# Kernel tuning notes

Hardware: AMD Instinct MI355X
Metric: run time of the kernel (lower is better)

Reference implementation:

```python
import jax, jax.numpy as jnp
import numpy as np

N_NODES = 65536
N_EDGES = 1048576
F_IN = 128
HEADS = 4
HID = 64
N_GRAPHS = 1024
NODES_PER_GRAPH = N_NODES // N_GRAPHS
EPS = 1e-5
NEG_SLOPE = 0.2


def setup_inputs() -> dict:
    key = jax.random.key(0)
    ks = jax.random.split(key, 8)
    x = jax.random.normal(ks[0], (N_NODES, F_IN), dtype=jnp.float32)
    edge_index = jax.random.randint(ks[1], (2, N_EDGES), 0, N_NODES, dtype=jnp.int64)
    batch = (jnp.arange(N_NODES, dtype=jnp.int64) // NODES_PER_GRAPH)
    s = 1.0 / np.sqrt(F_IN)
    w_l = jax.random.normal(ks[2], (HEADS * HID, F_IN), dtype=jnp.float32) * s
    w_r = jax.random.normal(ks[3], (HEADS * HID, F_IN), dtype=jnp.float32) * s
    att = jax.random.normal(ks[4], (HEADS, HID), dtype=jnp.float32) * (1.0 / np.sqrt(HID))
    return {
        "x": x,
        "edge_index": edge_index,
        "batch": batch,
        "num_graphs": N_GRAPHS,
        "bn_gamma": jnp.ones((F_IN,), jnp.float32),
        "bn_beta": jnp.zeros((F_IN,), jnp.float32),
        "w_l": w_l,
        "b_l": jnp.zeros((HEADS * HID,), jnp.float32),
        "w_r": w_r,
        "b_r": jnp.zeros((HEADS * HID,), jnp.float32),
        "att": att,
        "bias": jnp.zeros((HID,), jnp.float32),
    }


def reference(x, edge_index, batch, num_graphs, bn_gamma, bn_beta,
              w_l, b_l, w_r, b_r, att, bias):
    N = x.shape[0]
    H, C = att.shape
    # BatchNorm1d (training-mode: batch stats, biased variance)
    mean = jnp.mean(x, axis=0)
    var = jnp.var(x, axis=0)
    xn = (x - mean) * jax.lax.rsqrt(var + EPS) * bn_gamma + bn_beta
    # GATv2Conv: separate src/dst linear transforms
    xs = (xn @ w_l.T + b_l).reshape(N, H, C)
    xd = (xn @ w_r.T + b_r).reshape(N, H, C)
    # add self-loops (PyG default)
    loop = jnp.arange(N, dtype=edge_index.dtype)
    src = jnp.concatenate([edge_index[0], loop])
    dst = jnp.concatenate([edge_index[1], loop])
    # per-edge messages and GATv2 attention logits
    msg = xs[src]                               # [E, H, C]
    e = jax.nn.leaky_relu(msg + xd[dst], NEG_SLOPE)
    logits = jnp.einsum('ehc,hc->eh', e, att)    # [E, H]
    # segment-wise (per-destination) softmax
    m = jax.ops.segment_max(logits, dst, num_segments=N)
    p = jnp.exp(logits - m[dst])
    s = jax.ops.segment_sum(p, dst, num_segments=N)
    alpha = p / s[dst]                           # [E, H]
    # scatter-aggregate weighted messages
    out = jax.ops.segment_sum(alpha[:, :, None] * msg, dst, num_segments=N)  # [N,H,C]
    out = out.mean(axis=1) + bias                # concat=False -> mean over heads
    out = jax.nn.elu(out)
    return out.reshape(num_graphs, -1, C)
```

## Files before the change

### kernel.cpp

```cpp
#include <hip/hip_runtime.h>
#include <hip/hip_bf16.h>

#define N_NODES 65536
#define N_EDGES 1048576
#define F_IN    128
#define HEADS   4
#define HID     64
#define NHID    256
#define NBUCK   1024
#define BCAP    2048

typedef float fx4 __attribute__((ext_vector_type(4)));
typedef short bf16x8 __attribute__((ext_vector_type(8)));
typedef float f32x4 __attribute__((ext_vector_type(4)));

__device__ inline unsigned short f2bf(float f) {
    unsigned u = __float_as_uint(f);
    u += 0x7fff + ((u >> 16) & 1);
    return (unsigned short)(u >> 16);
}
__device__ inline float bf2f(unsigned short h) {
    return __uint_as_float((unsigned)h << 16);
}
__device__ inline float bflo(unsigned w) { return __uint_as_float(w << 16); }
__device__ inline float bfhi(unsigned w) { return __uint_as_float(w & 0xffff0000u); }

template <int CTRL>
__device__ inline float dpp_add(float x) {
    int y = __builtin_amdgcn_update_dpp(0, __float_as_int(x), CTRL, 0xf, 0xf, true);
    return x + __int_as_float(y);
}

__global__ __launch_bounds__(256) void k_bn_stats(const float* __restrict__ x,
                                                  float* __restrict__ sums,
                                                  unsigned short* __restrict__ xhi) {
    const int t = threadIdx.x;
    const int lane = t & 63;
    const int w = t >> 6;
    const int wid = blockIdx.x * 4 + w;
    float s0 = 0.f, s1 = 0.f, q0 = 0.f, q1 = 0.f;
    for (int i = 0; i < 64; ++i) {
        int r = wid + i * 1024;
        float2 v = *(const float2*)(x + (size_t)r * F_IN + lane * 2);
        s0 += v.x; q0 += v.x * v.x;
        s1 += v.y; q1 += v.y * v.y;
        unsigned short h0 = f2bf(v.x), h1 = f2bf(v.y);
        int slot = (lane >> 2) ^ (r & 7);
        int idx = r * 64 + slot * 4 + (lane & 3);
        ((unsigned*)xhi)[idx] = (unsigned)h0 | ((unsigned)h1 << 16);
    }
    __shared__ float sh[4][128];
    sh[w][lane * 2] = s0; sh[w][lane * 2 + 1] = s1;
    __syncthreads();
    if (t < 128) atomicAdd(&sums[t], sh[0][t] + sh[1][t] + sh[2][t] + sh[3][t]);
    __syncthreads();
    sh[w][lane * 2] = q0; sh[w][lane * 2 + 1] = q1;
    __syncthreads();
    if (t < 128) atomicAdd(&sums[128 + t], sh[0][t] + sh[1][t] + sh[2][t] + sh[3][t]);
}

__global__ void k_bn_finalize(const float* __restrict__ sums,
                              const float* __restrict__ gamma,
                              const float* __restrict__ beta,
                              const float* __restrict__ att,
                              float* __restrict__ scale,
                              float* __restrict__ shift,
                              float* __restrict__ att_l2e) {
    int t = threadIdx.x;
    float mean = sums[t] * (1.0f / N_NODES);
    float var  = sums[128 + t] * (1.0f / N_NODES) - mean * mean;
    float sc = gamma[t] * rsqrtf(var + 1e-5f);
    scale[t] = sc;
    shift[t] = beta[t] - mean * sc;
    att_l2e[t]       = att[t]       * 1.44269504088896f;
    att_l2e[t + 128] = att[t + 128] * 1.44269504088896f;
}

__global__ __launch_bounds__(256) void k_prep_w(const float* __restrict__ w_l,
                                                const float* __restrict__ b_l,
                                                const float* __restrict__ w_r,
                                                const float* __restrict__ b_r,
                                                const float* __restrict__ scale,
                                                const float* __restrict__ shift,
                                                unsigned short* __restrict__ Whi,
                                                unsigned short* __restrict__ Wlo,
                                                float* __restrict__ bp) {
    const int t = threadIdx.x;
    const int lane = t & 63;
    const int o = blockIdx.x * 4 + (t >> 6);
    const float* wrow = (o < NHID) ? (w_l + (size_t)o * F_IN)
                                   : (w_r + (size_t)(o - NHID) * F_IN);
    float bo = (o < NHID) ? b_l[o] : b_r[o - NHID];
    float2 wv = *(const float2*)(wrow + lane * 2);
    float w0 = wv.x * scale[lane * 2], w1 = wv.y * scale[lane * 2 + 1];
    unsigned short h0 = f2bf(w0), h1 = f2bf(w1);
    unsigned short l0 = f2bf(w0 - bf2f(h0)), l1 = f2bf(w1 - bf2f(h1));
    int slot = (lane >> 2) ^ (o & 7);
    int idx = o * 64 + slot * 4 + (lane & 3);
    ((unsigned*)Whi)[idx] = (unsigned)h0 | ((unsigned)h1 << 16);
    ((unsigned*)Wlo)[idx] = (unsigned)l0 | ((unsigned)l1 << 16);
    float part = shift[lane * 2] * wv.x + shift[lane * 2 + 1] * wv.y;
    #pragma unroll
    for (int m = 1; m < 64; m <<= 1) part += __shfl_xor(part, m, 64);
    if (lane == 0) bp[o] = bo + part;
}

__global__ __launch_bounds__(512) void k_gemm_mfma(const unsigned short* __restrict__ xhi,
                                                   const unsigned short* __restrict__ Whi,
                                                   const unsigned short* __restrict__ Wlo,
                                                   const float* __restrict__ bp,
                                                   unsigned short* __restrict__ xs_bf,
                                                   unsigned short* __restrict__ xd_bf) {
    __shared__ __align__(16) char lds[98304];
    const int t = threadIdx.x;
    const int bid = blockIdx.x;
    const int mb = (bid & 7) * 64 + ((bid >> 3) >> 2);
    const int nb = (bid >> 3) & 3;
    const int m0 = mb * 128, n0 = nb * 128;
    {
        const uint4* srcs[3] = {
            (const uint4*)(xhi + (size_t)m0 * 128),
            (const uint4*)(Whi + (size_t)n0 * 128),
            (const uint4*)(Wlo + (size_t)n0 * 128)};
        #pragma unroll
        for (int c = 0; c < 3; ++c) {
            uint4* dst = (uint4*)(lds + c * 32768);
            #pragma unroll
            for (int q = 0; q < 4; ++q) {
                int i = q * 512 + t;
                dst[i] = srcs[c][i];
            }
        }
    }
    __syncthreads();
    const int wvi = t >> 6, lane = t & 63;
    const int wm = wvi >> 2, wn = wvi & 3;
    const int lg = lane >> 4, lr = lane & 15;
    f32x4 acc[4][2] = {};
    #pragma unroll
    for (int ks = 0; ks < 4; ++ks) {
        bf16x8 ah[4], bh[2], bl[2];
        #pragma unroll
        for (int mi = 0; mi < 4; ++mi) {
            int r = wm * 64 + mi * 16 + lr;
            int off = r * 256 + ((((ks << 2) + lg) ^ (r & 7)) << 4);
            ah[mi] = *(const bf16x8*)(lds + off);
        }
        #pragma unroll
        for (int nj = 0; nj < 2; ++nj) {
            int r = wn * 32 + nj * 16 + lr;
            int off = r * 256 + ((((ks << 2) + lg) ^ (r & 7)) << 4);
            bh[nj] = *(const bf16x8*)(lds + 32768 + off);
            bl[nj] = *(const bf16x8*)(lds + 65536 + off);
        }
        #pragma unroll
        for (int mi = 0; mi < 4; ++mi)
            #pragma unroll
            for (int nj = 0; nj < 2; ++nj) {
                acc[mi][nj] = __builtin_amdgcn_mfma_f32_16x16x32_bf16(ah[mi], bh[nj], acc[mi][nj], 0, 0, 0);
                acc[mi][nj] = __builtin_amdgcn_mfma_f32_16x16x32_bf16(ah[mi], bl[nj], acc[mi][nj], 0, 0, 0);
            }
    }
    unsigned short* outp = (n0 < NHID) ? xs_bf : xd_bf;
    const int ncol0 = n0 & 255;
    #pragma unroll
    for (int nj = 0; nj < 2; ++nj) {
        int nc = wn * 32 + nj * 16 + lr;
        float bcol = bp[n0 + nc];
        #pragma unroll
        for (int mi = 0; mi < 4; ++mi) {
            #pragma unroll
            for (int r = 0; r < 4; ++r) {
                int m = m0 + wm * 64 + mi * 16 + lg * 4 + r;
                outp[(size_t)m * NHID + ncol0 + nc] = f2bf(acc[mi][nj][r] + bcol);
            }
        }
    }
}

__global__ __launch_bounds__(256) void k_coarse(const int* __restrict__ ei,
                                                int* __restrict__ ccnt,
                                                unsigned* __restrict__ cbuf) {
    __shared__ int cnt[NBUCK];
    __shared__ int base[NBUCK];
    const int t = threadIdx.x;
    for (int i = t; i < NBUCK; i += 256) cnt[i] = 0;
    __syncthreads();
    const int e0 = blockIdx.x * 4096;
    int myrank[16];
    #pragma unroll
    for (int k = 0; k < 16; ++k) {
        int d = ei[N_EDGES + e0 + k * 256 + t];
        myrank[k] = atomicAdd(&cnt[d >> 6], 1);
    }
    __syncthreads();
    for (int i = t; i < NBUCK; i += 256)
        base[i] = (i << 11) + atomicAdd(&ccnt[i], cnt[i]);
    __syncthreads();
    #pragma unroll
    for (int k = 0; k < 16; ++k) {
        int e = e0 + k * 256 + t;
        int s = ei[e];
        int d = ei[N_EDGES + e];
        unsigned pos = (unsigned)(base[d >> 6] + myrank[k]);
        if ((pos >> 11) == (unsigned)(d >> 6))
            cbuf[pos] = (unsigned)s | ((unsigned)(d & 63) << 16);
    }
}

__global__ __launch_bounds__(256) void k_fineA(const unsigned* __restrict__ cbuf,
                                               const int* __restrict__ ccnt,
                                               int* __restrict__ counts) {
    __shared__ int nc[64];
    const int t = threadIdx.x;
    const int b = blockIdx.x;
    if (t < 64) nc[t] = 0;
    __syncthreads();
    const int cnt = min(ccnt[b], BCAP);
    const unsigned* p = cbuf + (size_t)b * BCAP;
    for (int e = t; e < cnt; e += 256)
        atomicAdd(&nc[(p[e] >> 16) & 63], 1);
    __syncthreads();
    if (t < 64) counts[b * 64 + t] = nc[t];
}

__global__ __launch_bounds__(256) void k_scan1(const int* __restrict__ counts,
                                               int* __restrict__ row_start,
                                               int* __restrict__ blocksums) {
    __shared__ int sh[256];
    int t = threadIdx.x;
    int i = blockIdx.x * 256 + t;
    int v = counts[i];
    sh[t] = v;
    __syncthreads();
    for (int off = 1; off < 256; off <<= 1) {
        int add = (t >= off) ? sh[t - off] : 0;
        __syncthreads();
        sh[t] += add;
        __syncthreads();
    }
    row_start[i] = sh[t] - v;
    if (t == 255) blocksums[blockIdx.x] = sh[255];
}

__global__ void k_scan2(int* __restrict__ blocksums) {
    __shared__ int sh[256];
    int t = threadIdx.x;
    int v = blocksums[t];
    sh[t] = v;
    __syncthreads();
    for (int off = 1; off < 256; off <<= 1) {
        int add = (t >= off) ? sh[t - off] : 0;
        __syncthreads();
        sh[t] += add;
        __syncthreads();
    }
    blocksums[t] = sh[t] - v;
}

__global__ __launch_bounds__(256) void k_scan3(int* __restrict__ row_start,
                                               const int* __restrict__ blocksums) {
    int i = blockIdx.x * 256 + threadIdx.x;
    row_start[i] += blocksums[blockIdx.x];
}

__global__ __launch_bounds__(256) void k_fineB(const unsigned* __restrict__ cbuf,
                                               const int* __restrict__ ccnt,
                                               const int* __restrict__ row_start,
                                               int* __restrict__ csr) {
    __shared__ int rs[64];
    __shared__ int cur[64];
    const int t = threadIdx.x;
    const int b = blockIdx.x;
    if (t < 64) { rs[t] = row_start[b * 64 + t]; cur[t] = 0; }
    __syncthreads();
    const int cnt = min(ccnt[b], BCAP);
    const unsigned* p = cbuf + (size_t)b * BCAP;
    for (int e = t; e < cnt; e += 256) {
        unsigned w2 = p[e];
        int d = (w2 >> 16) & 63;
        int r = atomicAdd(&cur[d], 1);
        csr[rs[d] + r] = (int)(w2 & 0xffffu);
    }
}

__global__ __launch_bounds__(256, 4) void k_aggregate(const unsigned short* __restrict__ xs_bf,
                                                      const unsigned short* __restrict__ xd_bf,
                                                      const int* __restrict__ row_start,
                                                      const int* __restrict__ counts,
                                                      const int* __restrict__ csr,
                                                      const float* __restrict__ att_l2e,
                                                      const float* __restrict__ bias,
                                                      float* __restrict__ out) {
    const int t = threadIdx.x;
    const int lane = t & 63;
    const int q = lane & 31;
    const int h = lane >> 5;
    const int node  = __builtin_amdgcn_readfirstlane(blockIdx.x * 4 + (t >> 6));
    const int start = __builtin_amdgcn_readfirstlane(row_start[node]);
    const int deg   = __builtin_amdgcn_readfirstlane(counts[node]);
    const int total = deg + 1;
    const int* csrp = csr + start;

    float att8[8], xd8[8];
    {
        const float4* ap = (const float4*)(att_l2e + q * 8);
        float4 a0 = ap[0], a1 = ap[1];
        att8[0] = a0.x; att8[1] = a0.y; att8[2] = a0.z; att8[3] = a0.w;
        att8[4] = a1.x; att8[5] = a1.y; att8[6] = a1.z; att8[7] = a1.w;
        uint4 xw = *(const uint4*)(xd_bf + (size_t)node * NHID + q * 8);
        xd8[0] = bflo(xw.x); xd8[1] = bfhi(xw.x);
        xd8[2] = bflo(xw.y); xd8[3] = bfhi(xw.y);
        xd8[4] = bflo(xw.z); xd8[5] = bfhi(xw.z);
        xd8[6] = bflo(xw.w); xd8[7] = bfhi(xw.w);
    }

    const char* xsb = (const char*)xs_bf;
    const unsigned voff = (unsigned)q * 16;
    float ssum = 0.f;
    float acc[8] = {};

    int sA = node;
    int it1 = (1 < total) ? 1 : 0;
    int sB = (it1 == 0) ? node : csrp[it1 - 1];
    int srcv = h ? sB : sA;
    uint4 u = *(const uint4*)(xsb + (((unsigned)srcv << 9) | voff));

    for (int j = 0; j < total; j += 2) {
        uint4 cur = u;
        int jn = j + 2;
        if (jn < total) {
            int nA = csrp[jn - 1];
            int jB = (jn + 1 < total) ? jn + 1 : jn;
            int nB = csrp[jB - 1];
            int nsrc = h ? nB : nA;
            u = *(const uint4*)(xsb + (((unsigned)nsrc << 9) | voff));
        }
        float c0 = bflo(cur.x), c1 = bfhi(cur.x);
        float c2 = bflo(cur.y), c3 = bfhi(cur.y);
        float c4 = bflo(cur.z), c5 = bfhi(cur.z);
        float c6 = bflo(cur.w), c7 = bfhi(cur.w);
        float sv0 = c0 + xd8[0], sv1 = c1 + xd8[1];
        float sv2 = c2 + xd8[2], sv3 = c3 + xd8[3];
        float sv4 = c4 + xd8[4], sv5 = c5 + xd8[5];
        float sv6 = c6 + xd8[6], sv7 = c7 + xd8[7];
        float l0 = fmaxf(sv0, 0.2f * sv0), l1 = fmaxf(sv1, 0.2f * sv1);
        float l2 = fmaxf(sv2, 0.2f * sv2), l3 = fmaxf(sv3, 0.2f * sv3);
        float l4 = fmaxf(sv4, 0.2f * sv4), l5 = fmaxf(sv5, 0.2f * sv5);
        float l6 = fmaxf(sv6, 0.2f * sv6), l7 = fmaxf(sv7, 0.2f * sv7);
        float d = att8[0] * l0;
        d = fmaf(att8[1], l1, d); d = fmaf(att8[2], l2, d);
        d = fmaf(att8[3], l3, d); d = fmaf(att8[4], l4, d);
        d = fmaf(att8[5], l5, d); d = fmaf(att8[6], l6, d);
        d = fmaf(att8[7], l7, d);
        d = dpp_add<0xB1>(d);
        d = dpp_add<0x4E>(d);
        d = dpp_add<0x141>(d);
        if (j + h >= total) d = -1e30f;
        float p = __builtin_amdgcn_exp2f(d);
        ssum += p;
        acc[0] = fmaf(p, sv0, acc[0]); acc[1] = fmaf(p, sv1, acc[1]);
        acc[2] = fmaf(p, sv2, acc[2]); acc[3] = fmaf(p, sv3, acc[3]);
        acc[4] = fmaf(p, sv4, acc[4]); acc[5] = fmaf(p, sv5, acc[5]);
        acc[6] = fmaf(p, sv6, acc[6]); acc[7] = fmaf(p, sv7, acc[7]);
    }

    ssum += __shfl_xor(ssum, 32, 64);
    #pragma unroll
    for (int k = 0; k < 8; ++k) acc[k] += __shfl_xor(acc[k], 32, 64);
    float inv = __builtin_amdgcn_rcpf(ssum);
    float r[8];
    #pragma unroll
    for (int k = 0; k < 8; ++k) r[k] = fmaf(acc[k], inv, -xd8[k]);
    #pragma unroll
    for (int k = 0; k < 8; ++k) {
        r[k] += __shfl_xor(r[k], 8, 64);
        r[k] += __shfl_xor(r[k], 16, 64);
    }
    if (h == 0 && q < 8) {
        const float4* bp4 = (const float4*)(bias + q * 8);
        float4 b0 = bp4[0], b1 = bp4[1];
        float o[8];
        o[0] = r[0] * 0.25f + b0.x; o[1] = r[1] * 0.25f + b0.y;
        o[2] = r[2] * 0.25f + b0.z; o[3] = r[3] * 0.25f + b0.w;
        o[4] = r[4] * 0.25f + b1.x; o[5] = r[5] * 0.25f + b1.y;
        o[6] = r[6] * 0.25f + b1.z; o[7] = r[7] * 0.25f + b1.w;
        #pragma unroll
        for (int k = 0; k < 8; ++k) o[k] = (o[k] > 0.f) ? o[k] : expm1f(o[k]);
        float* op = out + (size_t)node * HID + q * 8;
        *(float4*)op       = {o[0], o[1], o[2], o[3]};
        *(float4*)(op + 4) = {o[4], o[5], o[6], o[7]};
    }
}

extern "C" void kernel_launch(void* const* d_in, const int* in_sizes, int n_in,
                              void* d_out, int out_size, void* d_ws, size_t ws_size,
                              hipStream_t stream) {
    const float* x     = (const float*)d_in[0];
    const int*   ei    = (const int*)d_in[1];
    const float* gamma = (const float*)d_in[4];
    const float* beta  = (const float*)d_in[5];
    const float* w_l   = (const float*)d_in[6];
    const float* b_l   = (const float*)d_in[7];
    const float* w_r   = (const float*)d_in[8];
    const float* b_r   = (const float*)d_in[9];
    const float* att   = (const float*)d_in[10];
    const float* bias  = (const float*)d_in[11];
    float* out = (float*)d_out;

    char* ws = (char*)d_ws;
    unsigned short* xs_bf = (unsigned short*)ws;
    unsigned short* xd_bf = xs_bf + (size_t)N_NODES * NHID;
    unsigned short* xhi   = xd_bf + (size_t)N_NODES * NHID;
    unsigned short* Whi   = xhi + (size_t)N_NODES * F_IN;
    unsigned short* Wlo   = Whi + 512 * F_IN;
    float* bp      = (float*)(Wlo + 512 * F_IN);
    float* scale   = bp + 512;
    float* shift   = scale + 128;
    float* att_l2e = shift + 128;
    float* sums    = att_l2e + 256;
    int* counts    = (int*)(sums + 256);
    int* ccnt      = counts + N_NODES;
    int* row_start = ccnt + NBUCK;
    int* blocksums = row_start + N_NODES;
    int* csr       = blocksums + 256;
    unsigned* cbuf = (unsigned*)(csr + N_EDGES);

    (void)hipMemsetAsync(sums, 0, (256 + N_NODES + NBUCK) * sizeof(float), stream);

    k_bn_stats<<<256, 256, 0, stream>>>(x, sums, xhi);
    k_bn_finalize<<<1, 128, 0, stream>>>(sums, gamma, beta, att, scale, shift, att_l2e);
    k_prep_w<<<128, 256, 0, stream>>>(w_l, b_l, w_r, b_r, scale, shift, Whi, Wlo, bp);
    k_gemm_mfma<<<2048, 512, 0, stream>>>(xhi, Whi, Wlo, bp, xs_bf, xd_bf);

    k_coarse<<<N_EDGES / 4096, 256, 0, stream>>>(ei, ccnt, cbuf);
    k_fineA<<<NBUCK, 256, 0, stream>>>(cbuf, ccnt, counts);
    k_scan1<<<256, 256, 0, stream>>>(counts, row_start, blocksums);
    k_scan2<<<1, 256, 0, stream>>>(blocksums);
    k_scan3<<<256, 256, 0, stream>>>(row_start, blocksums);
    k_fineB<<<NBUCK, 256, 0, stream>>>(cbuf, ccnt, row_start, csr);

    k_aggregate<<<N_NODES / 4, 256, 0, stream>>>(xs_bf, xd_bf, row_start, counts, csr,
                                                 att_l2e, bias, out);
}
```

Measured before the change: 180.5 us.

## Process one edge per wavefront with packed fp32 math and abs-based leaky-relu

Switches the aggregate kernel from two edges per wavefront (32 lanes x 8 features) to one edge per wavefront (64 lanes x 4 features), so edge gathers use 8-byte loads and no lanes are masked on odd degrees. Leaky-relu is rewritten algebraically as 0.6*x + 0.4*|x| (folded into the attention scale), and the accumulator now sums raw source features instead of source+destination, which drops the later xd subtraction. Math uses packed float2 vectors to target packed fp32 instructions, and ELU uses fast exp2 in place of expm1f. The trade-off is twice as many loop iterations per node and a longer dependent DPP reduction, with a small precision change in ELU.

```diff
diff --git a/kernel.cpp b/kernel.cpp
--- a/kernel.cpp
+++ b/kernel.cpp
@@ -13,6 +13,7 @@
 typedef float fx4 __attribute__((ext_vector_type(4)));
 typedef short bf16x8 __attribute__((ext_vector_type(8)));
 typedef float f32x4 __attribute__((ext_vector_type(4)));
+typedef float f32x2 __attribute__((ext_vector_type(2)));
 
 __device__ inline unsigned short f2bf(float f) {
     unsigned u = __float_as_uint(f);
@@ -284,112 +285,89 @@
     }
 }
 
-__global__ __launch_bounds__(256, 4) void k_aggregate(const unsigned short* __restrict__ xs_bf,
-                                                      const unsigned short* __restrict__ xd_bf,
-                                                      const int* __restrict__ row_start,
-                                                      const int* __restrict__ counts,
-                                                      const int* __restrict__ csr,
-                                                      const float* __restrict__ att_l2e,
-                                                      const float* __restrict__ bias,
-                                                      float* __restrict__ out) {
+__global__ __launch_bounds__(256) void k_aggregate(const unsigned short* __restrict__ xs_bf,
+                                                   const unsigned short* __restrict__ xd_bf,
+                                                   const int* __restrict__ row_start,
+                                                   const int* __restrict__ counts,
+                                                   const int* __restrict__ csr,
+                                                   const float* __restrict__ att_l2e,
+                                                   const float* __restrict__ bias,
+                                                   float* __restrict__ out) {
     const int t = threadIdx.x;
     const int lane = t & 63;
-    const int q = lane & 31;
-    const int h = lane >> 5;
     const int node  = __builtin_amdgcn_readfirstlane(blockIdx.x * 4 + (t >> 6));
     const int start = __builtin_amdgcn_readfirstlane(row_start[node]);
     const int deg   = __builtin_amdgcn_readfirstlane(counts[node]);
     const int total = deg + 1;
     const int* csrp = csr + start;
 
-    float att8[8], xd8[8];
+    f32x2 att01, att23, xd01, xd23;
     {
-        const float4* ap = (const float4*)(att_l2e + q * 8);
-        float4 a0 = ap[0], a1 = ap[1];
-        att8[0] = a0.x; att8[1] = a0.y; att8[2] = a0.z; att8[3] = a0.w;
-        att8[4] = a1.x; att8[5] = a1.y; att8[6] = a1.z; att8[7] = a1.w;
-        uint4 xw = *(const uint4*)(xd_bf + (size_t)node * NHID + q * 8);
-        xd8[0] = bflo(xw.x); xd8[1] = bfhi(xw.x);
-        xd8[2] = bflo(xw.y); xd8[3] = bfhi(xw.y);
-        xd8[4] = bflo(xw.z); xd8[5] = bfhi(xw.z);
-        xd8[6] = bflo(xw.w); xd8[7] = bfhi(xw.w);
+        float4 a = *(const float4*)(att_l2e + lane * 4);
+        att01.x = 0.6f * a.x; att01.y = 0.6f * a.y;
+        att23.x = 0.6f * a.z; att23.y = 0.6f * a.w;
+        uint2 xw = *(const uint2*)(xd_bf + (size_t)node * NHID + lane * 4);
+        xd01.x = bflo(xw.x); xd01.y = bfhi(xw.x);
+        xd23.x = bflo(xw.y); xd23.y = bfhi(xw.y);
     }
 
     const char* xsb = (const char*)xs_bf;
-    const unsigned voff = (unsigned)q * 16;
+    const unsigned voff = (unsigned)lane * 8;
     float ssum = 0.f;
-    float acc[8] = {};
-
-    int sA = node;
-    int it1 = (1 < total) ? 1 : 0;
-    int sB = (it1 == 0) ? node : csrp[it1 - 1];
-    int srcv = h ? sB : sA;
-    uint4 u = *(const uint4*)(xsb + (((unsigned)srcv << 9) | voff));
-
-    for (int j = 0; j < total; j += 2) {
-        uint4 cur = u;
-        int jn = j + 2;
-        if (jn < total) {
-            int nA = csrp[jn - 1];
-            int jB = (jn + 1 < total) ? jn + 1 : jn;
-            int nB = csrp[jB - 1];
-            int nsrc = h ? nB : nA;
-            u = *(const uint4*)(xsb + (((unsigned)nsrc << 9) | voff));
+    f32x2 acc01 = {0.f, 0.f}, acc23 = {0.f, 0.f};
+
+    int s1 = (total > 1) ? csrp[0] : node;
+    uint2 u0 = *(const uint2*)(xsb + (((size_t)(unsigned)node) << 9) + voff);
+    uint2 u1 = *(const uint2*)(xsb + (((size_t)(unsigned)s1) << 9) + voff);
+
+    for (int j = 0; j < total; ++j) {
+        uint2 cur = u0;
+        u0 = u1;
+        if (j + 2 < total) {
+            int sn = csrp[j + 1];
+            u1 = *(const uint2*)(xsb + (((size_t)(unsigned)sn) << 9) + voff);
         }
-        float c0 = bflo(cur.x), c1 = bfhi(cur.x);
-        float c2 = bflo(cur.y), c3 = bfhi(cur.y);
-        float c4 = bflo(cur.z), c5 = bfhi(cur.z);
-        float c6 = bflo(cur.w), c7 = bfhi(cur.w);
-        float sv0 = c0 + xd8[0], sv1 = c1 + xd8[1];
-        float sv2 = c2 + xd8[2], sv3 = c3 + xd8[3];
-        float sv4 = c4 + xd8[4], sv5 = c5 + xd8[5];
-        float sv6 = c6 + xd8[6], sv7 = c7 + xd8[7];
-        float l0 = fmaxf(sv0, 0.2f * sv0), l1 = fmaxf(sv1, 0.2f * sv1);
-        float l2 = fmaxf(sv2, 0.2f * sv2), l3 = fmaxf(sv3, 0.2f * sv3);
-        float l4 = fmaxf(sv4, 0.2f * sv4), l5 = fmaxf(sv5, 0.2f * sv5);
-        float l6 = fmaxf(sv6, 0.2f * sv6), l7 = fmaxf(sv7, 0.2f * sv7);
-        float d = att8[0] * l0;
-        d = fmaf(att8[1], l1, d); d = fmaf(att8[2], l2, d);
-        d = fmaf(att8[3], l3, d); d = fmaf(att8[4], l4, d);
-        d = fmaf(att8[5], l5, d); d = fmaf(att8[6], l6, d);
-        d = fmaf(att8[7], l7, d);
+        f32x2 c01, c23;
+        c01.x = bflo(cur.x); c01.y = bfhi(cur.x);
+        c23.x = bflo(cur.y); c23.y = bfhi(cur.y);
+        f32x2 sv01 = c01 + xd01;
+        f32x2 sv23 = c23 + xd23;
+        f32x2 dA2 = att01 * c01 + att23 * c23;
+        f32x2 a01, a23;
+        a01.x = fabsf(sv01.x); a01.y = fabsf(sv01.y);
+        a23.x = fabsf(sv23.x); a23.y = fabsf(sv23.y);
+        f32x2 dB2 = att01 * a01 + att23 * a23;
+        float d = fmaf(0.66666667f, dB2.x + dB2.y, dA2.x + dA2.y);
         d = dpp_add<0xB1>(d);
         d = dpp_add<0x4E>(d);
         d = dpp_add<0x141>(d);
-        if (j + h >= total) d = -1e30f;
+        d = dpp_add<0x140>(d);
         float p = __builtin_amdgcn_exp2f(d);
         ssum += p;
-        acc[0] = fmaf(p, sv0, acc[0]); acc[1] = fmaf(p, sv1, acc[1]);
-        acc[2] = fmaf(p, sv2, acc[2]); acc[3] = fmaf(p, sv3, acc[3]);
-        acc[4] = fmaf(p, sv4, acc[4]); acc[5] = fmaf(p, sv5, acc[5]);
-        acc[6] = fmaf(p, sv6, acc[6]); acc[7] = fmaf(p, sv7, acc[7]);
-    }
-
-    ssum += __shfl_xor(ssum, 32, 64);
-    #pragma unroll
-    for (int k = 0; k < 8; ++k) acc[k] += __shfl_xor(acc[k], 32, 64);
+        f32x2 p2 = {p, p};
+        acc01 += p2 * c01;
+        acc23 += p2 * c23;
+    }
+
     float inv = __builtin_amdgcn_rcpf(ssum);
-    float r[8];
-    #pragma unroll
-    for (int k = 0; k < 8; ++k) r[k] = fmaf(acc[k], inv, -xd8[k]);
-    #pragma unroll
-    for (int k = 0; k < 8; ++k) {
-        r[k] += __shfl_xor(r[k], 8, 64);
-        r[k] += __shfl_xor(r[k], 16, 64);
-    }
-    if (h == 0 && q < 8) {
-        const float4* bp4 = (const float4*)(bias + q * 8);
-        float4 b0 = bp4[0], b1 = bp4[1];
-        float o[8];
-        o[0] = r[0] * 0.25f + b0.x; o[1] = r[1] * 0.25f + b0.y;
-        o[2] = r[2] * 0.25f + b0.z; o[3] = r[3] * 0.25f + b0.w;
-        o[4] = r[4] * 0.25f + b1.x; o[5] = r[5] * 0.25f + b1.y;
-        o[6] = r[6] * 0.25f + b1.z; o[7] = r[7] * 0.25f + b1.w;
-        #pragma unroll
-        for (int k = 0; k < 8; ++k) o[k] = (o[k] > 0.f) ? o[k] : expm1f(o[k]);
-        float* op = out + (size_t)node * HID + q * 8;
-        *(float4*)op       = {o[0], o[1], o[2], o[3]};
-        *(float4*)(op + 4) = {o[4], o[5], o[6], o[7]};
+    float r0 = acc01.x * inv, r1 = acc01.y * inv;
+    float r2 = acc23.x * inv, r3 = acc23.y * inv;
+    r0 += __shfl_xor(r0, 16, 64); r0 += __shfl_xor(r0, 32, 64);
+    r1 += __shfl_xor(r1, 16, 64); r1 += __shfl_xor(r1, 32, 64);
+    r2 += __shfl_xor(r2, 16, 64); r2 += __shfl_xor(r2, 32, 64);
+    r3 += __shfl_xor(r3, 16, 64); r3 += __shfl_xor(r3, 32, 64);
+    if (lane < 16) {
+        float4 b4 = *(const float4*)(bias + lane * 4);
+        float o0 = r0 * 0.25f + b4.x;
+        float o1 = r1 * 0.25f + b4.y;
+        float o2 = r2 * 0.25f + b4.z;
+        float o3 = r3 * 0.25f + b4.w;
+        o0 = (o0 > 0.f) ? o0 : __builtin_amdgcn_exp2f(o0 * 1.44269504f) - 1.0f;
+        o1 = (o1 > 0.f) ? o1 : __builtin_amdgcn_exp2f(o1 * 1.44269504f) - 1.0f;
+        o2 = (o2 > 0.f) ? o2 : __builtin_amdgcn_exp2f(o2 * 1.44269504f) - 1.0f;
+        o3 = (o3 > 0.f) ? o3 : __builtin_amdgcn_exp2f(o3 * 1.44269504f) - 1.0f;
+        float4 o = {o0, o1, o2, o3};
+        *(float4*)(out + (size_t)node * HID + lane * 4) = o;
     }
 }
 
```

Result: slower. 192.5 us (+6.6%).
